# Kernel tuning notes

Hardware: AMD Instinct MI355X
Metric: run time of the kernel (lower is better)

The kernel has to match this reference:

```python
import jax, jax.numpy as jnp
import numpy as np

V, H, NH, FF, L = 30522, 768, 12, 3072, 2
B, S = 64, 128
EPS = 1e-12


def _ln(x, g, b):
    m = x.mean(-1, keepdims=True)
    v = jnp.var(x, axis=-1, keepdims=True)
    return (x - m) / jnp.sqrt(v + EPS) * g + b


def setup_inputs() -> dict:
    key = jax.random.key(0)
    ks = jax.random.split(key, 16)
    p = lambda k, shape: jax.random.normal(k, shape, jnp.float32) * 0.02
    return {
        "input_ids": jax.random.randint(ks[0], (B, S), 1, V).astype(jnp.int32),
        "token_type_ids": jnp.zeros((B, S), jnp.int32),
        "word_emb": p(ks[1], (V, H)),
        "pos_emb3": p(ks[2], (3, H)),
        "type_emb": p(ks[3], (2, H)),
        "emb_ln_g": jnp.ones((H,)), "emb_ln_b": jnp.zeros((H,)),
        "Wq": p(ks[4], (L, H, H)), "bq": jnp.zeros((L, H)),
        "Wk": p(ks[5], (L, H, H)), "bk": jnp.zeros((L, H)),
        "Wv": p(ks[6], (L, H, H)), "bv": jnp.zeros((L, H)),
        "Wo": p(ks[7], (L, H, H)), "bo": jnp.zeros((L, H)),
        "ln1_g": jnp.ones((L, H)), "ln1_b": jnp.zeros((L, H)),
        "W1": p(ks[8], (L, H, FF)), "b1": jnp.zeros((L, FF)),
        "W2": p(ks[9], (L, FF, H)), "b2": jnp.zeros((L, H)),
        "ln2_g": jnp.ones((L, H)), "ln2_b": jnp.zeros((L, H)),
        "Wg": p(ks[10], (H, H)), "bg": jnp.zeros((H,)),
        "pos_emb2": p(ks[11], (S, H)),
        "type_emb2": p(ks[12], (2, H)),
        "norm_g": jnp.ones((H,)), "norm_b": jnp.zeros((H,)),
    }


def _forward(input_ids, token_type_ids, word_emb, pos_emb3, type_emb,
             emb_ln_g, emb_ln_b, Wq, bq, Wk, bk, Wv, bv, Wo, bo,
             ln1_g, ln1_b, W1, b1, W2, b2, ln2_g, ln2_b,
             Wg, bg, pos_emb2, type_emb2, norm_g, norm_b):
    b, s = input_ids.shape
    # --- build trigram ids: row j = (prev, cur, next); one zero separator row per example ---
    prev = jnp.pad(input_ids, ((0, 0), (1, 0)))[:, :-1]
    nxt = jnp.pad(input_ids, ((0, 0), (0, 1)))[:, 1:]
    tri = jnp.stack([prev, input_ids, nxt], -1)                      # [B,S,3]
    tri = jnp.concatenate([tri, jnp.zeros((b, 1, 3), tri.dtype)], 1)  # [B,S+1,3]
    tri = tri.reshape(b * (s + 1), 3)                                # [N,3]
    mask = (tri > 0).astype(jnp.float32).at[:, 1].set(1.0)           # [N,3]
    bias = (1.0 - mask)[:, None, None, :] * -10000.0                 # extended attn mask

    # --- embeddings over trigram rows (token_type defaults to 0) ---
    x = word_emb[tri] + pos_emb3[None] + type_emb[0][None, None]
    x = _ln(x, emb_ln_g, emb_ln_b)

    dh = H // NH
    scale = float(1.0 / np.sqrt(dh))
    for i in range(L):  # shallow BERT layers, seq len = 3
        q = (x @ Wq[i] + bq[i]).reshape(-1, 3, NH, dh)
        k = (x @ Wk[i] + bk[i]).reshape(-1, 3, NH, dh)
        v = (x @ Wv[i] + bv[i]).reshape(-1, 3, NH, dh)
        scores = jnp.einsum('nqhd,nkhd->nhqk', q, k) * scale + bias
        a = jax.nn.softmax(scores, -1)
        c = jnp.einsum('nhqk,nkhd->nqhd', a, v).reshape(-1, 3, H)
        x = _ln(x + c @ Wo[i] + bo[i], ln1_g[i], ln1_b[i])
        f = jax.nn.gelu(x @ W1[i] + b1[i], approximate=False)
        x = _ln(x + f @ W2[i] + b2[i], ln2_g[i], ln2_b[i])

    # zero rows whose center token is padding, then sigmoid gate + mask
    center_ok = (tri[:, 1] > 0).astype(x.dtype)
    x = x * center_ok[:, None, None]
    x = x * jax.nn.sigmoid(x @ Wg + bg) * mask[..., None]

    # --- merge_ngrams: each token sums its 3 trigram appearances (vectorized shifted add) ---
    flat = x[:, 1]
    flat = flat.at[:-1].add(x[1:, 0]).at[1:].add(x[:-1, 2])
    hs = flat.reshape(b, s + 1, H)[:, :s]                            # drop separator rows

    aux = pos_emb2[None, :s] + type_emb2[token_type_ids]
    return _ln(hs + aux, norm_g, norm_b)


def reference(input_ids, token_type_ids, word_emb, pos_emb3, type_emb,
              emb_ln_g, emb_ln_b, Wq, bq, Wk, bk, Wv, bv, Wo, bo,
              ln1_g, ln1_b, W1, b1, W2, b2, ln2_g, ln2_b,
              Wg, bg, pos_emb2, type_emb2, norm_g, norm_b):
    return _forward(input_ids, token_type_ids, word_emb, pos_emb3, type_emb,
                    emb_ln_g, emb_ln_b, Wq, bq, Wk, bk, Wv, bv, Wo, bo,
                    ln1_g, ln1_b, W1, b1, W2, b2, ln2_g, ln2_b,
                    Wg, bg, pos_emb2, type_emb2, norm_g, norm_b)
```

## Files before the change

### kernel.cpp

```cpp
#include <hip/hip_runtime.h>
#include <math.h>

typedef unsigned short u16;
typedef unsigned int   u32;

#define H_    768
#define FF_   3072
#define L_    2
#define B_    64
#define S_    128
#define SP1   129
#define NROWS (B_*SP1)
#define M_    (NROWS*3)
#define MPAD  24832
#define MT_   (MPAD/128)
#define QKV_N 2304

typedef __attribute__((ext_vector_type(8))) short s16x8;
typedef __attribute__((ext_vector_type(4))) float f32x4;

__device__ __forceinline__ float bf2f(u16 u){ union{u32 i; float f;} c; c.i=((u32)u)<<16; return c.f; }
__device__ __forceinline__ u16 f2bf(float x){ union{float f; u32 i;} c; c.f=x; u32 r=c.i+0x7fffu+((c.i>>16)&1u); return (u16)(r>>16); }

__device__ __forceinline__ void bf4u(uint2 u, float* v){
  v[0]=bf2f((u16)(u.x&0xffffu)); v[1]=bf2f((u16)(u.x>>16));
  v[2]=bf2f((u16)(u.y&0xffffu)); v[3]=bf2f((u16)(u.y>>16));
}
__device__ __forceinline__ uint2 fpack4(const float* v){
  u32 lo=(u32)f2bf(v[0]) | ((u32)f2bf(v[1])<<16);
  u32 hi=(u32)f2bf(v[2]) | ((u32)f2bf(v[3])<<16);
  return make_uint2(lo,hi);
}
__device__ __forceinline__ float wredf(float v){
  #pragma unroll
  for (int o=32;o;o>>=1) v += __shfl_xor(v,o,64);
  return v;
}

typedef const __attribute__((address_space(1))) void* gas1_t;
typedef __attribute__((address_space(3))) void*       las3_t;
__device__ __forceinline__ void gload16(const void* g, void* l){
  __builtin_amdgcn_global_load_lds((gas1_t)g, (las3_t)l, 16, 0, 0);
}

struct TP9 { const float* s[9]; u16* d[9]; };

__global__ __launch_bounds__(256) void tconv_k(TP9 P, int Rr, int Cc){
  __shared__ u16 tle[32][33];
  const float* src = P.s[blockIdx.z];
  u16* dst = P.d[blockIdx.z];
  int c0 = blockIdx.x*32, r0 = blockIdx.y*32;
  int tx = threadIdx.x&31, ty = threadIdx.x>>5;
  #pragma unroll
  for (int i=0;i<32;i+=8) tle[ty+i][tx] = f2bf(src[(size_t)(r0+ty+i)*Cc + (c0+tx)]);
  __syncthreads();
  #pragma unroll
  for (int i=0;i<32;i+=8) dst[(size_t)(c0+ty+i)*Rr + (r0+tx)] = tle[tx][ty+i];
}

__global__ __launch_bounds__(256) void bcat_k(const float* bq, const float* bk, const float* bv, float* dst){
  int i = (int)(blockIdx.x*256u + threadIdx.x);
  if (i >= L_*QKV_N) return;
  int l = i/QKV_N, c = i - l*QKV_N;
  float v = (c<H_) ? bq[l*H_+c] : (c<2*H_) ? bk[l*H_+c-H_] : bv[l*H_+c-2*H_];
  dst[i] = v;
}

__global__ __launch_bounds__(256) void embed_k(const int* __restrict__ ids, const float* __restrict__ wemb,
    const float* __restrict__ pe3, const float* __restrict__ te, const float* __restrict__ gg,
    const float* __restrict__ bb, u16* __restrict__ x)
{
  int m = (int)((blockIdx.x*256u + threadIdx.x)>>6);
  int lane = threadIdx.x&63;
  size_t base = (size_t)m*H_;
  if (m >= M_){
    #pragma unroll
    for (int k3=0;k3<3;k3++){ int col=lane*4+k3*256; *(uint2*)&x[base+col]=make_uint2(0u,0u); }
    return;
  }
  int n = m/3, j = m - n*3;
  int bi = n/SP1, sp = n - bi*SP1;
  int id = 0;
  if (sp < S_){
    int s2 = sp + j - 1;
    if (s2 >= 0 && s2 < S_) id = ids[bi*S_ + s2];
  }
  const float* wr = wemb + (size_t)id*H_;
  const float* pr = pe3 + j*H_;
  float vals[12]; float s=0.f, sq=0.f;
  #pragma unroll
  for (int k3=0;k3<3;k3++){
    int col = lane*4 + k3*256;
    float4 wv = *(const float4*)(wr+col);
    float4 pv = *(const float4*)(pr+col);
    float4 tv = *(const float4*)(te+col);
    float a0=wv.x+pv.x+tv.x, a1=wv.y+pv.y+tv.y, a2=wv.z+pv.z+tv.z, a3=wv.w+pv.w+tv.w;
    vals[k3*4+0]=a0; vals[k3*4+1]=a1; vals[k3*4+2]=a2; vals[k3*4+3]=a3;
    s += a0+a1+a2+a3; sq += a0*a0+a1*a1+a2*a2+a3*a3;
  }
  s = wredf(s); sq = wredf(sq);
  float mean = s*(1.f/H_);
  float var  = sq*(1.f/H_) - mean*mean;
  float rstd = rsqrtf(fmaxf(var,0.f)+1e-12f);
  #pragma unroll
  for (int k3=0;k3<3;k3++){
    int col = lane*4 + k3*256;
    float o[4];
    #pragma unroll
    for (int t=0;t<4;t++) o[t] = (vals[k3*4+t]-mean)*rstd*gg[col+t] + bb[col+t];
    *(uint2*)&x[base+col] = fpack4(o);
  }
}

__global__ __launch_bounds__(256) void ln_k(const u16* __restrict__ in, const float* __restrict__ gg,
    const float* __restrict__ bb, u16* __restrict__ out)
{
  int row = (int)((blockIdx.x*256u + threadIdx.x)>>6);
  int lane = threadIdx.x&63;
  size_t base = (size_t)row*H_;
  float vals[12]; float s=0.f, sq=0.f;
  #pragma unroll
  for (int k3=0;k3<3;k3++){
    int col = lane*4+k3*256;
    float v[4]; bf4u(*(const uint2*)&in[base+col], v);
    #pragma unroll
    for (int t=0;t<4;t++){ vals[k3*4+t]=v[t]; s+=v[t]; sq+=v[t]*v[t]; }
  }
  s=wredf(s); sq=wredf(sq);
  float mean=s*(1.f/H_);
  float var=sq*(1.f/H_)-mean*mean;
  float rstd=rsqrtf(fmaxf(var,0.f)+1e-12f);
  #pragma unroll
  for (int k3=0;k3<3;k3++){
    int col=lane*4+k3*256;
    float o[4];
    #pragma unroll
    for (int t=0;t<4;t++) o[t]=(vals[k3*4+t]-mean)*rstd*gg[col+t]+bb[col+t];
    *(uint2*)&out[base+col]=fpack4(o);
  }
}

__global__ __launch_bounds__(256) void attn_k(u16* QKV)
{
  int gw = (int)((blockIdx.x*256u + threadIdx.x)>>6);
  int lane = threadIdx.x&63;
  int n = gw/12, h = gw - n*12;
  int sp = n % SP1;
  size_t base = (size_t)n*3*QKV_N + h*64 + lane;
  float q[3],k[3],v[3];
  #pragma unroll
  for (int j=0;j<3;j++){
    q[j]=bf2f(QKV[base+(size_t)j*QKV_N]);
    k[j]=bf2f(QKV[base+(size_t)j*QKV_N + H_]);
    v[j]=bf2f(QKV[base+(size_t)j*QKV_N + 2*H_]);
  }
  float sc[9];
  #pragma unroll
  for (int a=0;a<3;a++)
    #pragma unroll
    for (int b=0;b<3;b++) sc[a*3+b]=q[a]*k[b];
  #pragma unroll
  for (int o=32;o;o>>=1){
    #pragma unroll
    for (int t=0;t<9;t++) sc[t]+=__shfl_xor(sc[t],o,64);
  }
  float b0 = (sp>=1 && sp<S_) ? 0.f : -1e4f;
  float b2 = (sp<S_-1) ? 0.f : -1e4f;
  #pragma unroll
  for (int a=0;a<3;a++){
    float s0=sc[a*3+0]*0.125f+b0;
    float s1=sc[a*3+1]*0.125f;
    float s2=sc[a*3+2]*0.125f+b2;
    float mx=fmaxf(s0,fmaxf(s1,s2));
    float e0=expf(s0-mx), e1=expf(s1-mx), e2=expf(s2-mx);
    float cv=(e0*v[0]+e1*v[1]+e2*v[2])/(e0+e1+e2);
    QKV[base+(size_t)a*QKV_N]=f2bf(cv);
  }
}

template<int EPI>
__global__ __launch_bounds__(256,4) void gemm_k(const u16* __restrict__ A, int lda,
    const u16* __restrict__ Bt, const float* __restrict__ bias,
    const u16* __restrict__ R, int ldr, u16* __restrict__ C, int ldc, int K, int NT)
{
  __shared__ u16 As[2][4096];
  __shared__ u16 Bs[2][4096];
  const int tid = threadIdx.x;
  const int wave = tid>>6, lane = tid&63;
  const int wm = (wave>>1)*64, wn = (wave&1)*64;
  const int fr = lane&15, kg = lane>>4;

  const int nwg = (int)gridDim.x;
  const int qq = nwg>>3, rr = nwg&7;
  const int xcd = (int)blockIdx.x&7, idx = (int)blockIdx.x>>3;
  const int swz = (xcd<rr ? xcd*(qq+1) : rr*(qq+1) + (xcd-rr)*qq) + idx;
  const int bx = swz/NT, by = swz - bx*NT;

  f32x4 acc[4][4];
  #pragma unroll
  for (int i=0;i<4;i++)
    #pragma unroll
    for (int j=0;j<4;j++) acc[i][j] = (f32x4){0.f,0.f,0.f,0.f};

  const int ldab = lda*2, ldbb = K*2;
  const char* Ab = (const char*)(A + (size_t)bx*128*lda);
  const char* Bb = (const char*)(Bt + (size_t)by*128*K);
  const int s0r = tid>>2, s0c = (tid&3)*16;
  const int s1r = s0r + 64;
  const int wofs = wave*1024;

  auto stage = [&](int buf, int kt){
    const int kb = kt*64;
    char* ad = (char*)(&As[buf][0]) + wofs;
    char* bd = (char*)(&Bs[buf][0]) + wofs;
    gload16(Ab + (size_t)s0r*ldab + kb + s0c, ad);
    gload16(Ab + (size_t)s1r*ldab + kb + s0c, ad + 4096);
    gload16(Bb + (size_t)s0r*ldbb + kb + s0c, bd);
    gload16(Bb + (size_t)s1r*ldbb + kb + s0c, bd + 4096);
  };

  const int nt = K>>5;
  stage(0, 0);
  __syncthreads();
  int cur = 0;
  for (int t=0; t<nt; ++t){
    if (t+1 < nt) stage(cur^1, t+1);
    const char* AsB = (const char*)(&As[cur][0]);
    const char* BsB = (const char*)(&Bs[cur][0]);
    s16x8 af[4], bfr[4];
    #pragma unroll
    for (int i=0;i<4;i++) af[i]  = *(const s16x8*)(AsB + ((wm+i*16+fr)<<6) + (kg<<4));
    #pragma unroll
    for (int j=0;j<4;j++) bfr[j] = *(const s16x8*)(BsB + ((wn+j*16+fr)<<6) + (kg<<4));
    __builtin_amdgcn_s_setprio(1);
    #pragma unroll
    for (int i=0;i<4;i++)
      #pragma unroll
      for (int j=0;j<4;j++)
        acc[i][j] = __builtin_amdgcn_mfma_f32_16x16x32_bf16(af[i], bfr[j], acc[i][j], 0,0,0);
    __builtin_amdgcn_s_setprio(0);
    __syncthreads();
    cur ^= 1;
  }

  const int gr0 = bx*128 + wm + (lane>>4)*4;
  const int gc0 = by*128 + wn + fr;
  #pragma unroll
  for (int j=0;j<4;j++){
    const int col = gc0 + j*16;
    const float bc = bias[col];
    #pragma unroll
    for (int i=0;i<4;i++){
      #pragma unroll
      for (int r=0;r<4;r++){
        const int row = gr0 + i*16 + r;
        float v = acc[i][j][r] + bc;
        if (EPI==1) v += bf2f(R[(size_t)row*ldr + col]);
        if (EPI==2) v = 0.5f*v*(1.f+erff(v*0.70710678118654752f));
        if (EPI==3){
          float xv = bf2f(R[(size_t)row*ldr + col]);
          int nn = row/3, j3 = row - nn*3;
          int sp = nn % SP1;
          float mk = (j3==1) ? 1.f : ((j3==0) ? (((sp>=1)&&(sp<S_))?1.f:0.f) : ((sp<S_-1)?1.f:0.f));
          v = xv * (1.f/(1.f+expf(-v))) * mk;
        }
        C[(size_t)row*ldc + col] = f2bf(v);
      }
    }
  }
}

__global__ __launch_bounds__(256) void final_k(const u16* __restrict__ G, const int* __restrict__ tt,
    const float* __restrict__ pe2, const float* __restrict__ te2, const float* __restrict__ gg,
    const float* __restrict__ bb, float* __restrict__ out)
{
  int r = (int)((blockIdx.x*256u+threadIdx.x)>>6);
  int lane = threadIdx.x&63;
  int bi = r>>7, sp = r&127;
  int n = bi*SP1+sp;
  int t = tt[r];
  size_t g1 = ((size_t)n*3+1)*H_;
  size_t g0 = ((size_t)(n+1)*3+0)*H_;
  size_t g2 = (n>0) ? ((size_t)(n-1)*3+2)*H_ : 0;
  const float* p2 = pe2 + (size_t)sp*H_;
  const float* t2 = te2 + (size_t)t*H_;
  float vals[12]; float s=0.f, sq=0.f;
  #pragma unroll
  for (int k3=0;k3<3;k3++){
    int col=lane*4+k3*256;
    float a[4], b[4], c[4]={0.f,0.f,0.f,0.f};
    bf4u(*(const uint2*)&G[g1+col], a);
    bf4u(*(const uint2*)&G[g0+col], b);
    if (n>0) bf4u(*(const uint2*)&G[g2+col], c);
    #pragma unroll
    for (int q=0;q<4;q++){
      float v = a[q]+b[q]+c[q] + p2[col+q] + t2[col+q];
      vals[k3*4+q]=v; s+=v; sq+=v*v;
    }
  }
  s=wredf(s); sq=wredf(sq);
  float mean=s*(1.f/H_), var=sq*(1.f/H_)-mean*mean;
  float rstd=rsqrtf(fmaxf(var,0.f)+1e-12f);
  #pragma unroll
  for (int k3=0;k3<3;k3++){
    int col=lane*4+k3*256;
    float4 o;
    o.x=(vals[k3*4+0]-mean)*rstd*gg[col+0]+bb[col+0];
    o.y=(vals[k3*4+1]-mean)*rstd*gg[col+1]+bb[col+1];
    o.z=(vals[k3*4+2]-mean)*rstd*gg[col+2]+bb[col+2];
    o.w=(vals[k3*4+3]-mean)*rstd*gg[col+3]+bb[col+3];
    *(float4*)&out[(size_t)r*H_+col]=o;
  }
}

extern "C" void kernel_launch(void* const* d_in, const int* in_sizes, int n_in,
                              void* d_out, int out_size, void* d_ws, size_t ws_size,
                              hipStream_t stream)
{
  (void)in_sizes; (void)n_in; (void)out_size;
  const int*   ids  = (const int*)d_in[0];
  const int*   tt   = (const int*)d_in[1];
  const float* wemb = (const float*)d_in[2];
  const float* pe3  = (const float*)d_in[3];
  const float* te   = (const float*)d_in[4];
  const float* elg  = (const float*)d_in[5];
  const float* elb  = (const float*)d_in[6];
  const float* Wq   = (const float*)d_in[7];
  const float* bq   = (const float*)d_in[8];
  const float* Wk   = (const float*)d_in[9];
  const float* bk   = (const float*)d_in[10];
  const float* Wv   = (const float*)d_in[11];
  const float* bv   = (const float*)d_in[12];
  const float* Wo   = (const float*)d_in[13];
  const float* bo   = (const float*)d_in[14];
  const float* l1g  = (const float*)d_in[15];
  const float* l1b  = (const float*)d_in[16];
  const float* W1   = (const float*)d_in[17];
  const float* b1   = (const float*)d_in[18];
  const float* W2   = (const float*)d_in[19];
  const float* b2   = (const float*)d_in[20];
  const float* l2g  = (const float*)d_in[21];
  const float* l2b  = (const float*)d_in[22];
  const float* Wg   = (const float*)d_in[23];
  const float* bg   = (const float*)d_in[24];
  const float* pe2  = (const float*)d_in[25];
  const float* te2  = (const float*)d_in[26];
  const float* ng   = (const float*)d_in[27];
  const float* nb   = (const float*)d_in[28];

  char* p = (char*)d_ws;
  auto alloc = [&](size_t bytes)->char*{
    char* r = p; p += (bytes + 255) & ~((size_t)255); return r;
  };
  const size_t HH = (size_t)H_*H_;
  u16*  wqkv = (u16*)alloc((size_t)L_*3*HH*2);
  u16*  wto  = (u16*)alloc((size_t)L_*HH*2);
  u16*  wt1  = (u16*)alloc((size_t)L_*H_*FF_*2);
  u16*  wt2  = (u16*)alloc((size_t)L_*H_*FF_*2);
  u16*  wtg  = (u16*)alloc(HH*2);
  float* bqkv= (float*)alloc((size_t)L_*QKV_N*4);
  u16*  xb   = (u16*)alloc((size_t)MPAD*H_*2);
  u16*  qkv  = (u16*)alloc((size_t)MPAD*QKV_N*2);
  u16*  kbf  = (u16*)alloc((size_t)MPAD*H_*2);
  size_t used = (size_t)(p - (char*)d_ws);
  size_t avail = ws_size > used ? ws_size - used : 0;
  long long mrows = (long long)(avail / ((size_t)FF_*2));
  int strip = (int)((mrows/128)*128);
  if (strip > MPAD) strip = MPAD;
  if (strip < 128) strip = 128;
  u16* fbf = (u16*)alloc((size_t)strip*FF_*2);

  {
    TP9 P;
    P.s[0]=Wq;     P.d[0]=wqkv;
    P.s[1]=Wk;     P.d[1]=wqkv+HH;
    P.s[2]=Wv;     P.d[2]=wqkv+2*HH;
    P.s[3]=Wq+HH;  P.d[3]=wqkv+3*HH;
    P.s[4]=Wk+HH;  P.d[4]=wqkv+4*HH;
    P.s[5]=Wv+HH;  P.d[5]=wqkv+5*HH;
    P.s[6]=Wo;     P.d[6]=wto;
    P.s[7]=Wo+HH;  P.d[7]=wto+HH;
    P.s[8]=Wg;     P.d[8]=wtg;
    tconv_k<<<dim3(H_/32, H_/32, 9), 256, 0, stream>>>(P, H_, H_);
  }
  {
    TP9 P; for (int i=0;i<9;i++){P.s[i]=Wq;P.d[i]=wtg;}
    P.s[0]=W1;                 P.d[0]=wt1;
    P.s[1]=W1+(size_t)H_*FF_;  P.d[1]=wt1+(size_t)H_*FF_;
    tconv_k<<<dim3(FF_/32, H_/32, 2), 256, 0, stream>>>(P, H_, FF_);
  }
  {
    TP9 P; for (int i=0;i<9;i++){P.s[i]=Wq;P.d[i]=wtg;}
    P.s[0]=W2;                 P.d[0]=wt2;
    P.s[1]=W2+(size_t)H_*FF_;  P.d[1]=wt2+(size_t)H_*FF_;
    tconv_k<<<dim3(H_/32, FF_/32, 2), 256, 0, stream>>>(P, FF_, H_);
  }
  bcat_k<<<(L_*QKV_N+255)/256, 256, 0, stream>>>(bq, bk, bv, bqkv);

  embed_k<<<MPAD/4, 256, 0, stream>>>(ids, wemb, pe3, te, elg, elb, xb);

  for (int i=0;i<L_;i++){
    const u16* wqkv_i = wqkv + (size_t)i*3*HH;
    const u16* wo_i   = wto  + (size_t)i*HH;
    const u16* w1_i   = wt1  + (size_t)i*H_*FF_;
    const u16* w2_i   = wt2  + (size_t)i*H_*FF_;
    gemm_k<0><<<MT_*18,256,0,stream>>>(xb, H_, wqkv_i, bqkv+(size_t)i*QKV_N,
                                       (const u16*)0, 0, qkv, QKV_N, H_, 18);
    attn_k<<<(NROWS*12)/4, 256, 0, stream>>>(qkv);
    gemm_k<1><<<MT_*6,256,0,stream>>>(qkv, QKV_N, wo_i, bo+(size_t)i*H_, xb, H_, kbf, H_, H_, 6);
    ln_k<<<M_/4,256,0,stream>>>(kbf, l1g+(size_t)i*H_, l1b+(size_t)i*H_, xb);
    for (int s0=0; s0<MPAD; s0+=strip){
      int rows = MPAD - s0; if (rows > strip) rows = strip;
      gemm_k<2><<<(rows/128)*24,256,0,stream>>>(xb+(size_t)s0*H_, H_, w1_i, b1+(size_t)i*FF_,
                                                (const u16*)0, 0, fbf, FF_, H_, 24);
      gemm_k<1><<<(rows/128)*6,256,0,stream>>>(fbf, FF_, w2_i, b2+(size_t)i*H_,
                                               xb+(size_t)s0*H_, H_, kbf+(size_t)s0*H_, H_, FF_, 6);
    }
    ln_k<<<M_/4,256,0,stream>>>(kbf, l2g+(size_t)i*H_, l2b+(size_t)i*H_, xb);
  }
  gemm_k<3><<<MT_*6,256,0,stream>>>(xb, H_, wtg, bg, xb, H_, kbf, H_, H_, 6);
  final_k<<<(B_*S_)/4, 256, 0, stream>>>(kbf, tt, pe2, te2, ng, nb, (float*)d_out);
}
```

Baseline: 1.739 ms.

## Replace 128x128 GEMM with 256x256 tile, 8-wave kernel using swizzled LDS and pipelining

Every GEMM now runs in a new kernel with 512 threads computing a 256x256 output tile. It holds 64KB of bf16 A and B tiles in LDS, with an XOR swizzle on the column offset to avoid bank conflicts. Global loads are interleaved at fine grain across eight phases per iteration, with vmcnt waits and raw barriers. The aim is more data reuse per load and better overlap of loads with MFMA compute. The cost is higher register and LDS use, lower occupancy, and fewer workgroups for the small-N GEMMs.

```diff
diff --git a/kernel.cpp b/kernel.cpp
--- a/kernel.cpp
+++ b/kernel.cpp
@@ -13,7 +13,6 @@
 #define NROWS (B_*SP1)
 #define M_    (NROWS*3)
 #define MPAD  24832
-#define MT_   (MPAD/128)
 #define QKV_N 2304
 
 typedef __attribute__((ext_vector_type(8))) short s16x8;
@@ -179,15 +178,15 @@
 }
 
 template<int EPI>
-__global__ __launch_bounds__(256,4) void gemm_k(const u16* __restrict__ A, int lda,
+__global__ __launch_bounds__(512,2) void gemm256_k(const u16* __restrict__ A, int lda,
     const u16* __restrict__ Bt, const float* __restrict__ bias,
     const u16* __restrict__ R, int ldr, u16* __restrict__ C, int ldc, int K, int NT)
 {
-  __shared__ u16 As[2][4096];
-  __shared__ u16 Bs[2][4096];
+  __shared__ u16 Als[32768];
+  __shared__ u16 Bls[32768];
   const int tid = threadIdx.x;
-  const int wave = tid>>6, lane = tid&63;
-  const int wm = (wave>>1)*64, wn = (wave&1)*64;
+  const int wid = tid>>6, lane = tid&63;
+  const int wr = wid>>2, wc = wid&3;
   const int fr = lane&15, kg = lane>>4;
 
   const int nwg = (int)gridDim.x;
@@ -196,65 +195,95 @@
   const int swz = (xcd<rr ? xcd*(qq+1) : rr*(qq+1) + (xcd-rr)*qq) + idx;
   const int bx = swz/NT, by = swz - bx*NT;
 
-  f32x4 acc[4][4];
-  #pragma unroll
-  for (int i=0;i<4;i++)
+  f32x4 acc[8][4];
+  #pragma unroll
+  for (int i=0;i<8;i++)
     #pragma unroll
     for (int j=0;j<4;j++) acc[i][j] = (f32x4){0.f,0.f,0.f,0.f};
 
   const int ldab = lda*2, ldbb = K*2;
-  const char* Ab = (const char*)(A + (size_t)bx*128*lda);
-  const char* Bb = (const char*)(Bt + (size_t)by*128*K);
-  const int s0r = tid>>2, s0c = (tid&3)*16;
-  const int s1r = s0r + 64;
-  const int wofs = wave*1024;
-
-  auto stage = [&](int buf, int kt){
-    const int kb = kt*64;
-    char* ad = (char*)(&As[buf][0]) + wofs;
-    char* bd = (char*)(&Bs[buf][0]) + wofs;
-    gload16(Ab + (size_t)s0r*ldab + kb + s0c, ad);
-    gload16(Ab + (size_t)s1r*ldab + kb + s0c, ad + 4096);
-    gload16(Bb + (size_t)s0r*ldbb + kb + s0c, bd);
-    gload16(Bb + (size_t)s1r*ldbb + kb + s0c, bd + 4096);
+  const char* Ab = (const char*)(A + (size_t)bx*256*lda);
+  const char* Bb = (const char*)(Bt + (size_t)by*256*K);
+  char* AlsB = (char*)Als; char* BlsB = (char*)Bls;
+
+  const int r0 = tid>>2;
+  const int c_sw = ((tid&3)*16) ^ (((r0>>1)&3)<<4);
+  const int wdst = wid<<10;
+
+  auto stA = [&](int tile, int kh){
+    char* d = AlsB + ((((tile&1)<<1)|kh)<<14) + wdst;
+    const char* s = Ab + (size_t)r0*ldab + tile*128 + kh*64 + c_sw;
+    gload16(s, d);
+    gload16(s + (size_t)128*ldab, d + 8192);
   };
-
-  const int nt = K>>5;
-  stage(0, 0);
-  __syncthreads();
-  int cur = 0;
-  for (int t=0; t<nt; ++t){
-    if (t+1 < nt) stage(cur^1, t+1);
-    const char* AsB = (const char*)(&As[cur][0]);
-    const char* BsB = (const char*)(&Bs[cur][0]);
-    s16x8 af[4], bfr[4];
-    #pragma unroll
-    for (int i=0;i<4;i++) af[i]  = *(const s16x8*)(AsB + ((wm+i*16+fr)<<6) + (kg<<4));
-    #pragma unroll
-    for (int j=0;j<4;j++) bfr[j] = *(const s16x8*)(BsB + ((wn+j*16+fr)<<6) + (kg<<4));
-    __builtin_amdgcn_s_setprio(1);
-    #pragma unroll
-    for (int i=0;i<4;i++)
+  auto stB = [&](int tile, int kh){
+    char* d = BlsB + ((((tile&1)<<1)|kh)<<14) + wdst;
+    const char* s = Bb + (size_t)r0*ldbb + tile*128 + kh*64 + c_sw;
+    gload16(s, d);
+    gload16(s + (size_t)128*ldbb, d + 8192);
+  };
+
+  const int nt = K>>6;
+  const int niter = nt>>1;
+
+  stA(0,0); stB(0,0); stA(0,1); stB(0,1); stA(1,0); stB(1,0);
+  asm volatile("s_waitcnt vmcnt(8)" ::: "memory");
+  __builtin_amdgcn_s_barrier();
+
+  for (int i=0; i<niter; ++i){
+    const bool last = (i == niter-1);
+    #pragma unroll
+    for (int p=0; p<8; ++p){
+      const int Tloc = p>>2;
+      const int T = 2*i + Tloc;
+      const int kk = (p>>1)&1;
+      const int mh = p&1;
+      const char* sA = AlsB + (((Tloc<<1)|kk)<<14);
+      const char* sB = BlsB + (((Tloc<<1)|kk)<<14);
+      s16x8 af[4], bfv[4];
       #pragma unroll
-      for (int j=0;j<4;j++)
-        acc[i][j] = __builtin_amdgcn_mfma_f32_16x16x32_bf16(af[i], bfr[j], acc[i][j], 0,0,0);
-    __builtin_amdgcn_s_setprio(0);
-    __syncthreads();
-    cur ^= 1;
-  }
-
-  const int gr0 = bx*128 + wm + (lane>>4)*4;
-  const int gc0 = by*128 + wn + fr;
-  #pragma unroll
-  for (int j=0;j<4;j++){
-    const int col = gc0 + j*16;
+      for (int f=0; f<4; ++f){
+        const int row = wr*128 + mh*64 + f*16 + fr;
+        af[f] = *(const s16x8*)(sA + (row<<6) + ((kg<<4) ^ (((row>>1)&3)<<4)));
+      }
+      #pragma unroll
+      for (int g=0; g<4; ++g){
+        const int col = wc*64 + g*16 + fr;
+        bfv[g] = *(const s16x8*)(sB + (col<<6) + ((kg<<4) ^ (((col>>1)&3)<<4)));
+      }
+      const int j = p&3;
+      if (j==0){ const int t2=T+1; if (t2<nt) stA(t2,1); }
+      else if (j==1){ const int t2=T+1; if (t2<nt) stB(t2,1); }
+      else if (j==2){ const int t2=T+2; if (t2<nt) stA(t2,0); }
+      else          { const int t2=T+2; if (t2<nt) stB(t2,0); }
+      __builtin_amdgcn_s_barrier();
+      __builtin_amdgcn_s_setprio(1);
+      #pragma unroll
+      for (int f=0; f<4; ++f)
+        #pragma unroll
+        for (int g=0; g<4; ++g)
+          acc[mh*4+f][g] = __builtin_amdgcn_mfma_f32_16x16x32_bf16(af[f], bfv[g], acc[mh*4+f][g], 0,0,0);
+      __builtin_amdgcn_s_setprio(0);
+      if (p&1){
+        if (last) { asm volatile("s_waitcnt vmcnt(0)" ::: "memory"); }
+        else      { asm volatile("s_waitcnt vmcnt(8)" ::: "memory"); }
+      }
+      __builtin_amdgcn_s_barrier();
+    }
+  }
+
+  const int gr0 = bx*256 + wr*128 + (lane>>4)*4;
+  const int gc0 = by*256 + wc*64 + fr;
+  #pragma unroll
+  for (int g=0; g<4; ++g){
+    const int col = gc0 + g*16;
     const float bc = bias[col];
     #pragma unroll
-    for (int i=0;i<4;i++){
+    for (int mi=0; mi<8; ++mi){
       #pragma unroll
-      for (int r=0;r<4;r++){
-        const int row = gr0 + i*16 + r;
-        float v = acc[i][j][r] + bc;
+      for (int r=0; r<4; ++r){
+        const int row = gr0 + mi*16 + r;
+        float v = acc[mi][g][r] + bc;
         if (EPI==1) v += bf2f(R[(size_t)row*ldr + col]);
         if (EPI==2) v = 0.5f*v*(1.f+erff(v*0.70710678118654752f));
         if (EPI==3){
@@ -365,9 +394,9 @@
   size_t used = (size_t)(p - (char*)d_ws);
   size_t avail = ws_size > used ? ws_size - used : 0;
   long long mrows = (long long)(avail / ((size_t)FF_*2));
-  int strip = (int)((mrows/128)*128);
+  int strip = (int)((mrows/256)*256);
   if (strip > MPAD) strip = MPAD;
-  if (strip < 128) strip = 128;
+  if (strip < 256) strip = 256;
   u16* fbf = (u16*)alloc((size_t)strip*FF_*2);
 
   {
@@ -399,25 +428,26 @@
 
   embed_k<<<MPAD/4, 256, 0, stream>>>(ids, wemb, pe3, te, elg, elb, xb);
 
+  const int NBX = MPAD/256;
   for (int i=0;i<L_;i++){
     const u16* wqkv_i = wqkv + (size_t)i*3*HH;
     const u16* wo_i   = wto  + (size_t)i*HH;
     const u16* w1_i   = wt1  + (size_t)i*H_*FF_;
     const u16* w2_i   = wt2  + (size_t)i*H_*FF_;
-    gemm_k<0><<<MT_*18,256,0,stream>>>(xb, H_, wqkv_i, bqkv+(size_t)i*QKV_N,
-                                       (const u16*)0, 0, qkv, QKV_N, H_, 18);
+    gemm256_k<0><<<NBX*9,512,0,stream>>>(xb, H_, wqkv_i, bqkv+(size_t)i*QKV_N,
+                                         (const u16*)0, 0, qkv, QKV_N, H_, 9);
     attn_k<<<(NROWS*12)/4, 256, 0, stream>>>(qkv);
-    gemm_k<1><<<MT_*6,256,0,stream>>>(qkv, QKV_N, wo_i, bo+(size_t)i*H_, xb, H_, kbf, H_, H_, 6);
+    gemm256_k<1><<<NBX*3,512,0,stream>>>(qkv, QKV_N, wo_i, bo+(size_t)i*H_, xb, H_, kbf, H_, H_, 3);
     ln_k<<<M_/4,256,0,stream>>>(kbf, l1g+(size_t)i*H_, l1b+(size_t)i*H_, xb);
     for (int s0=0; s0<MPAD; s0+=strip){
       int rows = MPAD - s0; if (rows > strip) rows = strip;
-      gemm_k<2><<<(rows/128)*24,256,0,stream>>>(xb+(size_t)s0*H_, H_, w1_i, b1+(size_t)i*FF_,
-                                                (const u16*)0, 0, fbf, FF_, H_, 24);
-      gemm_k<1><<<(rows/128)*6,256,0,stream>>>(fbf, FF_, w2_i, b2+(size_t)i*H_,
-                                               xb+(size_t)s0*H_, H_, kbf+(size_t)s0*H_, H_, FF_, 6);
+      gemm256_k<2><<<(rows/256)*12,512,0,stream>>>(xb+(size_t)s0*H_, H_, w1_i, b1+(size_t)i*FF_,
+                                                   (const u16*)0, 0, fbf, FF_, H_, 12);
+      gemm256_k<1><<<(rows/256)*3,512,0,stream>>>(fbf, FF_, w2_i, b2+(size_t)i*H_,
+                                                  xb+(size_t)s0*H_, H_, kbf+(size_t)s0*H_, H_, FF_, 3);
     }
     ln_k<<<M_/4,256,0,stream>>>(kbf, l2g+(size_t)i*H_, l2b+(size_t)i*H_, xb);
   }
-  gemm_k<3><<<MT_*6,256,0,stream>>>(xb, H_, wtg, bg, xb, H_, kbf, H_, H_, 6);
+  gemm256_k<3><<<NBX*3,512,0,stream>>>(xb, H_, wtg, bg, xb, H_, kbf, H_, H_, 3);
   final_k<<<(B_*S_)/4, 256, 0, stream>>>(kbf, tt, pe2, te2, ng, nb, (float*)d_out);
 }
```

New measurement: 1.916 ms. 10.2% more time.
